# Performance work log

Hardware: AMD Instinct MI355X
Metric: run time of the kernel (lower is better)

Reference implementation:

```python
import jax, jax.numpy as jnp
import numpy as np

D_MODEL = 1024
B, T_Q, T_KV = 4, 2048, 2048


def _linear_params(key, d_in, d_out):
    kw, kb = jax.random.split(key)
    W = jax.random.normal(kw, (d_out, d_in), dtype=jnp.float32) * 0.02
    b = jax.random.normal(kb, (d_out,), dtype=jnp.float32) * 0.02
    return W, b


def setup_inputs() -> dict:
    key = jax.random.key(0)
    ks = jax.random.split(key, 7)
    latent_space = jax.random.normal(ks[0], (B, T_Q, D_MODEL), dtype=jnp.float32)
    input_space = jax.random.normal(ks[1], (B, T_KV, D_MODEL), dtype=jnp.float32)
    Wl, bl = _linear_params(ks[2], D_MODEL, D_MODEL)
    Wu, bu = _linear_params(ks[3], D_MODEL, D_MODEL)
    WA, bA = _linear_params(ks[4], D_MODEL, D_MODEL)  # A_proj: d -> J (J = d)
    WV, bV = _linear_params(ks[5], D_MODEL, D_MODEL)  # V_proj: J -> d
    Wo, bo = _linear_params(ks[6], D_MODEL, D_MODEL)
    return {
        "latent_space": latent_space, "input_space": input_space,
        "Wl": Wl, "bl": bl, "Wu": Wu, "bu": bu,
        "WA": WA, "bA": bA, "WV": WV, "bV": bV,
        "Wo": Wo, "bo": bo,
    }


def reference(latent_space, input_space, Wl, bl, Wu, bu, WA, bA, WV, bV, Wo, bo):
    # emb_0 = l_proj(latent)            [B, T_q, d]
    emb0 = jnp.einsum('bqd,ed->bqe', latent_space, Wl) + bl
    # l = softmax(u_proj(emb_0), -1)^T  [B, d, T_q]
    l = jax.nn.softmax(jnp.einsum('bqd,ed->bqe', emb0, Wu) + bu, axis=-1)
    l = jnp.swapaxes(l, -2, -1)
    # D = A_proj(input)                 [B, T_kv, J]
    Dm = jnp.einsum('bkd,jd->bkj', input_space, WA) + bA
    # A = softmax(V_proj(D), dim=-2)    softmax over T_kv
    A = jax.nn.softmax(jnp.einsum('bkj,dj->bkd', Dm, WV) + bV, axis=-2)
    # w = A @ l                         [B, T_kv, T_q]
    w = jnp.einsum('bkd,bdq->bkq', A, l)
    # o = w @ o_proj(latent)            [B, T_kv, d]
    ov = jnp.einsum('bqd,ed->bqe', latent_space, Wo) + bo
    o = jnp.einsum('bkq,bqd->bkd', w, ov)
    return o
```

## Files before the change

kernel.cpp:

```cpp
#include <hip/hip_runtime.h>
#include <hip/hip_bf16.h>
#include <stdint.h>

typedef __attribute__((ext_vector_type(8))) short bf16x8;
typedef __attribute__((ext_vector_type(4))) float f32x4;
typedef __attribute__((ext_vector_type(4))) unsigned short u16x4;

#define B_  4
#define T_  2048
#define D_  1024
#define BM  128
#define BN  128
#define BK  32

__device__ __forceinline__ float bf2f(ushort u) {
  union { unsigned int i; float f; } v; v.i = ((unsigned int)u) << 16; return v.f;
}
__device__ __forceinline__ ushort f2bf(float f) {
  return (ushort)(__bfloat16_as_ushort(__float2bfloat16(f)));
}
__device__ __forceinline__ void async16(const void* g, void* l) {
  __builtin_amdgcn_global_load_lds(
      (const __attribute__((address_space(1))) void*)g,
      (__attribute__((address_space(3))) void*)l, 16, 0, 0);
}
__device__ __forceinline__ int swz4(int r) { return (r ^ (r >> 2)) & 3; }

__global__ __launch_bounds__(256)
void prep(const float* __restrict__ lat, const float* __restrict__ inp,
          const float* __restrict__ Wl, const float* __restrict__ bl,
          const float* __restrict__ Wu, const float* __restrict__ bu,
          const float* __restrict__ WA, const float* __restrict__ bA,
          const float* __restrict__ WV, const float* __restrict__ bV,
          const float* __restrict__ Wo, const float* __restrict__ bo,
          ushort* __restrict__ xBf, ushort* __restrict__ xBf2,
          ushort* __restrict__ w1, ushort* __restrict__ w2,
          ushort* __restrict__ wCatWo, float* __restrict__ bc, float* __restrict__ bc2)
{
  __shared__ alignas(16) ushort t[64 * 65];
  const long NW = (long)D_ * D_;
  const int bx = blockIdx.x;
  const int tid = threadIdx.x;
  if (bx < 16384) {
    const float* in = bx < 8192 ? lat : inp;
    ushort* out = bx < 8192 ? xBf : xBf2;
    const long i = (long)(bx & 8191) * 256 + tid;
    const float4 v = *(const float4*)(in + i * 4);
    u16x4 o;
    o[0] = f2bf(v.x); o[1] = f2bf(v.y); o[2] = f2bf(v.z); o[3] = f2bf(v.w);
    *(u16x4*)(out + i * 4) = o;
  } else if (bx < 19456) {
    const int seg = (bx - 16384) >> 10;
    const float* in  = seg == 0 ? Wu : (seg == 1 ? WV : Wo);
    ushort* out = seg == 0 ? w1 : (seg == 1 ? w1 + NW : wCatWo);
    const long i = (long)((bx - 16384) & 1023) * 256 + tid;
    const float4 v = *(const float4*)(in + i * 4);
    u16x4 o;
    o[0] = f2bf(v.x); o[1] = f2bf(v.y); o[2] = f2bf(v.z); o[3] = f2bf(v.w);
    *(u16x4*)(out + i * 4) = o;
  } else if (bx < 19968) {
    const int z = (bx - 19456) >> 8;
    const int w = (bx - 19456) & 255;
    const float* in = z ? WA : Wl;
    ushort* out = z ? w2 + NW : w2;
    const int c0 = (w & 15) * 64, r0 = (w >> 4) * 64;
    const int tx = tid & 15, ty = tid >> 4;
#pragma unroll
    for (int i = 0; i < 4; ++i) {
      const int r = ty + i * 16;
      const float4 v = *(const float4*)(in + (long)(r0 + r) * D_ + c0 + tx * 4);
      t[(tx * 4 + 0) * 65 + r] = f2bf(v.x);
      t[(tx * 4 + 1) * 65 + r] = f2bf(v.y);
      t[(tx * 4 + 2) * 65 + r] = f2bf(v.z);
      t[(tx * 4 + 3) * 65 + r] = f2bf(v.w);
    }
    __syncthreads();
#pragma unroll
    for (int i = 0; i < 4; ++i) {
      const int c = ty + i * 16;
      u16x4 v;
#pragma unroll
      for (int j = 0; j < 4; ++j) v[j] = t[c * 65 + tx * 4 + j];
      *(u16x4*)(out + (long)(c0 + c) * D_ + r0 + tx * 4) = v;
    }
  } else {
    const int z = (bx - 19968) >> 8;
    const int w = (bx - 19968) & 255;
    const float* W    = z ? WV : Wu;
    const float* bin  = z ? bA : bl;
    const float* badd = z ? bV : bu;
    float* out        = z ? bc2 : bc;
    const int wv = tid >> 6, lane = tid & 63;
    const int e = w * 4 + wv;
    const float* row = W + (long)e * D_;
    float s = 0.f;
#pragma unroll
    for (int i = 0; i < 16; ++i) s += row[lane + i * 64] * bin[lane + i * 64];
#pragma unroll
    for (int off = 32; off; off >>= 1) s += __shfl_xor(s, off);
    if (lane == 0) out[e] = s + badd[e];
  }
}

template<bool OUT_F32, bool HAS_BIAS, bool EXP_OUT>
__global__ __launch_bounds__(256, 2)
void gemm_nt(const ushort* __restrict__ A, const ushort* __restrict__ B,
             const float* __restrict__ bias, void* __restrict__ C,
             int N, int K, long sA, long sB, long sC)
{
  __shared__ alignas(16) ushort As[BM * BK];
  __shared__ alignas(16) ushort Bs[BN * BK];
  const int tid  = threadIdx.x;
  const int wave = tid >> 6;
  const int lane = tid & 63;
  const int wm   = wave >> 1;
  const int wn   = wave & 1;
  const int bz   = blockIdx.z;
  const int tileN = blockIdx.x * BN;
  const int tileM = blockIdx.y * BM;
  A += (long)bz * sA;
  B += (long)bz * sB;

  const int lrow   = lane >> 2;
  const int lchunk = (lane & 3) ^ swz4(lrow);

  f32x4 acc[4][4];
#pragma unroll
  for (int i = 0; i < 4; ++i)
#pragma unroll
    for (int j = 0; j < 4; ++j) acc[i][j] = (f32x4){0.f, 0.f, 0.f, 0.f};

  const int frow = lane & 15;
  const int kg   = lane >> 4;
  const int coff = ((kg ^ swz4(frow)) << 3);

  for (int kt = 0; kt < K; kt += BK) {
    __syncthreads();
#pragma unroll
    for (int i = 0; i < 2; ++i) {
      const int rg  = wave * 2 + i;
      const int row = rg * 16 + lrow;
      async16(A + (long)(tileM + row) * K + kt + lchunk * 8, (void*)(As + rg * 16 * BK));
      async16(B + (long)(tileN + row) * K + kt + lchunk * 8, (void*)(Bs + rg * 16 * BK));
    }
    __syncthreads();
    bf16x8 af[4], bfr[4];
#pragma unroll
    for (int mi = 0; mi < 4; ++mi)
      af[mi] = *(const bf16x8*)(As + (wm * 64 + mi * 16 + frow) * BK + coff);
#pragma unroll
    for (int ni = 0; ni < 4; ++ni)
      bfr[ni] = *(const bf16x8*)(Bs + (wn * 64 + ni * 16 + frow) * BK + coff);
#pragma unroll
    for (int mi = 0; mi < 4; ++mi)
#pragma unroll
      for (int ni = 0; ni < 4; ++ni)
        acc[mi][ni] = __builtin_amdgcn_mfma_f32_16x16x32_bf16(af[mi], bfr[ni], acc[mi][ni], 0, 0, 0);
  }

  const int rowbase = tileM + wm * 64 + ((lane >> 4) << 2);
  const int colbase = tileN + wn * 64 + (lane & 15);
#pragma unroll
  for (int ni = 0; ni < 4; ++ni) {
    const int col = colbase + ni * 16;
    float bv = 0.f;
    if constexpr (HAS_BIAS) bv = bias[col];
#pragma unroll
    for (int mi = 0; mi < 4; ++mi) {
#pragma unroll
      for (int r = 0; r < 4; ++r) {
        const int row = rowbase + mi * 16 + r;
        float v = acc[mi][ni][r] + bv;
        if constexpr (EXP_OUT) v = __expf(v);
        const long idx = (long)bz * sC + (long)row * N + col;
        if constexpr (OUT_F32) ((float*)C)[idx] = v;
        else ((ushort*)C)[idx] = f2bf(v);
      }
    }
  }
}

__global__ __launch_bounds__(512, 2)
void gemm256(const ushort* __restrict__ A, const ushort* __restrict__ Bm,
             const float* __restrict__ bias1, const float* __restrict__ bias2,
             ushort* __restrict__ C1, ushort* __restrict__ C2,
             int ldA, int ldB)
{
  __shared__ alignas(16) ushort AbS[2 * 16384];
  __shared__ alignas(16) ushort BbS[2 * 16384];

  const int gx = gridDim.x, gy = gridDim.y;
  const int nwg = gx * gy;
  int fid = blockIdx.y * gx + blockIdx.x;
  fid = (fid & 7) * (nwg >> 3) + (fid >> 3);
  const int bx = fid % gx;
  const int by = fid / gx;
  const int tileM = by * 256, tileN = bx * 256;

  const int tid  = threadIdx.x;
  const int wid  = tid >> 6;
  const int lane = tid & 63;
  const int wm   = wid >> 2;
  const int wn   = wid & 3;

  const int srow = tid >> 2;
  const int sc   = (((tid & 3) ^ ((tid >> 3) & 3)) << 3);
  const ushort* gA[2] = { A  + (long)(tileM + srow) * ldA + sc,
                          A  + (long)(tileM + 128 + srow) * ldA + sc };
  const ushort* gB[2] = { Bm + (long)(tileN + srow) * ldB + sc,
                          Bm + (long)(tileN + 128 + srow) * ldB + sc };
  const int dofs = tid << 3;

  const int frow = lane & 15;
  const int cofs = (((lane >> 4) ^ ((lane >> 1) & 3)) << 3);
  int aoff[8], boff[4];
#pragma unroll
  for (int f = 0; f < 8; ++f) {
    const int r = wm * 64 + (f & 3) * 16 + frow;
    aoff[f] = ((f >> 2) << 13) + (r << 5) + cofs;
  }
#pragma unroll
  for (int n = 0; n < 4; ++n) {
    const int row = wn * 64 + n * 16 + frow;
    boff[n] = ((row >> 7) << 13) + ((row & 127) << 5) + cofs;
  }

#define STA256(b, h, kh, kt) async16(gA[h] + (long)(kt) * 64 + (kh) * 32, \
    AbS + (b) * 16384 + (h) * 8192 + (kh) * 4096 + dofs)
#define STB256(b, h, kh, kt) async16(gB[h] + (long)(kt) * 64 + (kh) * 32, \
    BbS + (b) * 16384 + (h) * 8192 + (kh) * 4096 + dofs)

  f32x4 acc[8][4];
#pragma unroll
  for (int i = 0; i < 8; ++i)
#pragma unroll
    for (int j = 0; j < 4; ++j) acc[i][j] = (f32x4){0.f, 0.f, 0.f, 0.f};

#pragma unroll
  for (int p = 0; p < 2; ++p) {
    STA256(p, 0, 0, p); STA256(p, 0, 1, p); STA256(p, 1, 0, p); STA256(p, 1, 1, p);
    STB256(p, 0, 0, p); STB256(p, 0, 1, p); STB256(p, 1, 0, p); STB256(p, 1, 1, p);
  }
  asm volatile("s_waitcnt vmcnt(0)" ::: "memory");
  __builtin_amdgcn_s_barrier();

#pragma unroll 1
  for (int t = 0; t < 16; ++t) {
    const int buf = t & 1;
    const ushort* Ac = AbS + buf * 16384;
    const ushort* Bc = BbS + buf * 16384;
    bf16x8 fa[4], fb[4];

#pragma unroll
    for (int n = 0; n < 4; ++n) fb[n] = *(const bf16x8*)(Bc + boff[n]);
#pragma unroll
    for (int f = 0; f < 4; ++f) fa[f] = *(const bf16x8*)(Ac + aoff[f]);
    if (t == 15) asm volatile("s_waitcnt vmcnt(0)" ::: "memory");
    else         asm volatile("s_waitcnt vmcnt(6)" ::: "memory");
    __builtin_amdgcn_s_barrier();
    __builtin_amdgcn_sched_barrier(0);
    if (t >= 1 && t <= 14) { STA256(buf ^ 1, 1, 0, t + 1); STA256(buf ^ 1, 1, 1, t + 1); }
    __builtin_amdgcn_s_setprio(1);
#pragma unroll
    for (int f = 0; f < 4; ++f)
#pragma unroll
      for (int n = 0; n < 4; ++n)
        acc[f][n] = __builtin_amdgcn_mfma_f32_16x16x32_bf16(fa[f], fb[n], acc[f][n], 0, 0, 0);
    __builtin_amdgcn_s_setprio(0);

    bf16x8 ga[4];
#pragma unroll
    for (int f = 0; f < 4; ++f) ga[f] = *(const bf16x8*)(Ac + aoff[4 + f]);
    __builtin_amdgcn_s_setprio(1);
#pragma unroll
    for (int f = 0; f < 4; ++f)
#pragma unroll
      for (int n = 0; n < 4; ++n)
        acc[4 + f][n] = __builtin_amdgcn_mfma_f32_16x16x32_bf16(ga[f], fb[n], acc[4 + f][n], 0, 0, 0);
    __builtin_amdgcn_s_setprio(0);

#pragma unroll
    for (int n = 0; n < 4; ++n) fb[n] = *(const bf16x8*)(Bc + boff[n] + 4096);
#pragma unroll
    for (int f = 0; f < 4; ++f) fa[f] = *(const bf16x8*)(Ac + aoff[f] + 4096);
    __builtin_amdgcn_s_setprio(1);
#pragma unroll
    for (int f = 0; f < 4; ++f)
#pragma unroll
      for (int n = 0; n < 4; ++n)
        acc[f][n] = __builtin_amdgcn_mfma_f32_16x16x32_bf16(fa[f], fb[n], acc[f][n], 0, 0, 0);
    __builtin_amdgcn_s_setprio(0);

#pragma unroll
    for (int f = 0; f < 4; ++f) ga[f] = *(const bf16x8*)(Ac + aoff[4 + f] + 4096);
    if (t >= 1 && t <= 14) asm volatile("s_waitcnt vmcnt(2)" ::: "memory");
    __builtin_amdgcn_s_barrier();
    __builtin_amdgcn_sched_barrier(0);
    if (t <= 13) {
      STA256(buf, 0, 0, t + 2); STA256(buf, 0, 1, t + 2);
      STB256(buf, 0, 0, t + 2); STB256(buf, 0, 1, t + 2);
      STB256(buf, 1, 0, t + 2); STB256(buf, 1, 1, t + 2);
    }
    __builtin_amdgcn_s_setprio(1);
#pragma unroll
    for (int f = 0; f < 4; ++f)
#pragma unroll
      for (int n = 0; n < 4; ++n)
        acc[4 + f][n] = __builtin_amdgcn_mfma_f32_16x16x32_bf16(ga[f], fb[n], acc[4 + f][n], 0, 0, 0);
    __builtin_amdgcn_s_setprio(0);
  }
#undef STA256
#undef STB256

  const bool second = tileN >= 1024;
  ushort* Cp = second ? C2 : C1;
  const float* bb = second ? bias2 : bias1;
  const int cb = tileN - (second ? 1024 : 0) + wn * 64 + (lane & 15);
#pragma unroll
  for (int mi = 0; mi < 8; ++mi) {
    const int mrow = tileM + wm * 64 + ((mi & 3) << 4) + ((mi >> 2) << 7) + ((lane >> 4) << 2);
#pragma unroll
    for (int ni = 0; ni < 4; ++ni) {
      const int col = cb + ni * 16;
      const float bv = bb[col];
#pragma unroll
      for (int r = 0; r < 4; ++r)
        Cp[(long)(mrow + r) * 1024 + col] = f2bf(acc[mi][ni][r] + bv);
    }
  }
}

template<int MODE>
__global__ __launch_bounds__(512, 2)
void gemm128(const ushort* __restrict__ A, const ushort* __restrict__ Bm,
             const float* __restrict__ bias1, void* __restrict__ C1,
             int ldA, int ldB, long sAz, long sBz, long sCz)
{
  __shared__ alignas(16) ushort AbS[3 * 16384];
  __shared__ alignas(16) ushort BbS[3 * 8192];

  const int gx = gridDim.x, gy = gridDim.y;
  const int nwg = gx * gy * gridDim.z;
  int fid = (blockIdx.z * gy + blockIdx.y) * gx + blockIdx.x;
  fid = (fid & 7) * (nwg >> 3) + (fid >> 3);
  const int bx = fid % gx;
  const int by = (fid / gx) % gy;
  const int bz = fid / (gx * gy);
  const int tileM = by * 256, tileN = bx * 128;

  const ushort* Ap = A;
  const ushort* Bp = Bm;
  if constexpr (MODE == 2) {
    Ap += (long)(bz >> 1) * sAz + (long)(bz & 1) * 1024;
    Bp += (long)(bz >> 1) * sBz + (long)(bz & 1) * 1024;
  } else {
    Ap += (long)bz * sAz;
    Bp += (long)bz * sBz;
  }

  const int tid  = threadIdx.x;
  const int wid  = tid >> 6;
  const int lane = tid & 63;
  const int wm   = wid >> 1;
  const int wn   = wid & 1;

  const int srow = tid >> 2;
  const int sc   = (((tid & 3) ^ ((tid >> 3) & 3)) << 3);
  const ushort* gA[2] = { Ap + (long)(tileM + srow) * ldA + sc,
                          Ap + (long)(tileM + 128 + srow) * ldA + sc };
  const ushort* gB    =   Bp + (long)(tileN + srow) * ldB + sc;
  const int dofs = tid << 3;

  const int frow = lane & 15;
  const int cofs = (((lane >> 4) ^ ((lane >> 1) & 3)) << 3);
  int aoff[4], boff[4];
#pragma unroll
  for (int f = 0; f < 4; ++f) {
    const int row = wm * 64 + f * 16 + frow;
    aoff[f] = ((row >> 7) << 13) + ((row & 127) << 5) + cofs;
  }
#pragma unroll
  for (int n = 0; n < 4; ++n) {
    const int row = wn * 64 + n * 16 + frow;
    boff[n] = (row << 5) + cofs;
  }

#define STA128(b, h, kh, kt) async16(gA[h] + (long)(kt) * 64 + (kh) * 32, \
    AbS + (b) * 16384 + (h) * 8192 + (kh) * 4096 + dofs)
#define STB128(b, kh, kt) async16(gB + (long)(kt) * 64 + (kh) * 32, \
    BbS + (b) * 8192 + (kh) * 4096 + dofs)
#define STAGE_TILE(b, kt) { STA128(b, 0, 0, kt); STA128(b, 0, 1, kt); \
    STA128(b, 1, 0, kt); STA128(b, 1, 1, kt); STB128(b, 0, kt); STB128(b, 1, kt); }

  f32x4 acc[4][4];
#pragma unroll
  for (int i = 0; i < 4; ++i)
#pragma unroll
    for (int j = 0; j < 4; ++j) acc[i][j] = (f32x4){0.f, 0.f, 0.f, 0.f};

  STAGE_TILE(0, 0);
  STAGE_TILE(1, 1);
  asm volatile("s_waitcnt vmcnt(0)" ::: "memory");
  __builtin_amdgcn_s_barrier();

#pragma unroll 1
  for (int t = 0; t < 16; ++t) {
    const int buf = t - (t / 3) * 3;
    const int nb  = (t + 2) - ((t + 2) / 3) * 3;
    const ushort* Ac = AbS + buf * 16384;
    const ushort* Bc = BbS + buf * 8192;
    bf16x8 fa[4], fb[4];

#pragma unroll
    for (int n = 0; n < 4; ++n) fb[n] = *(const bf16x8*)(Bc + boff[n]);
#pragma unroll
    for (int f = 0; f < 4; ++f) fa[f] = *(const bf16x8*)(Ac + aoff[f]);
    __builtin_amdgcn_s_barrier();
    __builtin_amdgcn_sched_barrier(0);
    if (t <= 13) STAGE_TILE(nb, t + 2);
    __builtin_amdgcn_s_setprio(1);
#pragma unroll
    for (int f = 0; f < 4; ++f)
#pragma unroll
      for (int n = 0; n < 4; ++n)
        acc[f][n] = __builtin_amdgcn_mfma_f32_16x16x32_bf16(fa[f], fb[n], acc[f][n], 0, 0, 0);
    __builtin_amdgcn_s_setprio(0);

#pragma unroll
    for (int n = 0; n < 4; ++n) fb[n] = *(const bf16x8*)(Bc + boff[n] + 4096);
#pragma unroll
    for (int f = 0; f < 4; ++f) fa[f] = *(const bf16x8*)(Ac + aoff[f] + 4096);
    if (t <= 13)      asm volatile("s_waitcnt vmcnt(6)" ::: "memory");
    else if (t == 14) asm volatile("s_waitcnt vmcnt(0)" ::: "memory");
    __builtin_amdgcn_s_barrier();
    __builtin_amdgcn_sched_barrier(0);
    __builtin_amdgcn_s_setprio(1);
#pragma unroll
    for (int f = 0; f < 4; ++f)
#pragma unroll
      for (int n = 0; n < 4; ++n)
        acc[f][n] = __builtin_amdgcn_mfma_f32_16x16x32_bf16(fa[f], fb[n], acc[f][n], 0, 0, 0);
    __builtin_amdgcn_s_setprio(0);
  }
#undef STA128
#undef STB128
#undef STAGE_TILE

  const int cb = tileN + wn * 64 + (lane & 15);
  const int rb = tileM + wm * 64 + ((lane >> 4) << 2);

  if constexpr (MODE == 1) {
    ushort* Cp = (ushort*)C1;
#pragma unroll
    for (int ni = 0; ni < 4; ++ni) {
      const int col = cb + ni * 16;
      const float bv = bias1[col];
#pragma unroll
      for (int mi = 0; mi < 4; ++mi)
#pragma unroll
        for (int r = 0; r < 4; ++r)
          Cp[(long)(rb + mi * 16 + r) * 1024 + col] = f2bf(__expf(acc[mi][ni][r] + bv));
    }
  } else if constexpr (MODE == 2) {
    ushort* Cp = (ushort*)C1 + ((long)(bz & 1) * B_ + (bz >> 1)) * ((long)D_ * D_);
#pragma unroll
    for (int ni = 0; ni < 4; ++ni) {
      const int col = cb + ni * 16;
#pragma unroll
      for (int mi = 0; mi < 4; ++mi)
#pragma unroll
        for (int r = 0; r < 4; ++r)
          Cp[(long)(rb + mi * 16 + r) * 1024 + col] = f2bf(acc[mi][ni][r]);
    }
  } else {
    float* Cp = (float*)C1 + (long)bz * sCz;
#pragma unroll
    for (int ni = 0; ni < 4; ++ni) {
      const int col = cb + ni * 16;
#pragma unroll
      for (int mi = 0; mi < 4; ++mi)
#pragma unroll
        for (int r = 0; r < 4; ++r)
          Cp[(long)(rb + mi * 16 + r) * 1024 + col] = acc[mi][ni][r];
    }
  }
}

__global__ __launch_bounds__(256)
void reduce2_scale(const ushort* __restrict__ P, const float* __restrict__ cinv,
                   ushort* __restrict__ MT)
{
  const long stride = (long)B_ * D_ * D_;
  const long base = ((long)blockIdx.x * 256 + threadIdx.x) * 8;
  const int b = (int)(base >> 20);
  const int e0 = (int)(base & (D_ - 1));
  bf16x8 p0 = *(const bf16x8*)(P + base);
  bf16x8 p1 = *(const bf16x8*)(P + stride + base);
  const float4 c0 = *(const float4*)(cinv + (long)b * D_ + e0);
  const float4 c1 = *(const float4*)(cinv + (long)b * D_ + e0 + 4);
  const float cc[8] = {c0.x, c0.y, c0.z, c0.w, c1.x, c1.y, c1.z, c1.w};
  bf16x8 o;
#pragma unroll
  for (int j = 0; j < 8; ++j)
    o[j] = (short)f2bf((bf2f((ushort)p0[j]) + bf2f((ushort)p1[j])) * cc[j]);
  *(bf16x8*)(MT + base) = o;
}

__global__ __launch_bounds__(256)
void softmax_row(ushort* __restrict__ S)
{
  const long base = (long)blockIdx.x * D_;
  const int tid = threadIdx.x;
  float e[4], s = 0.f;
#pragma unroll
  for (int i = 0; i < 4; ++i) { e[i] = __expf(bf2f(S[base + i * 256 + tid])); s += e[i]; }
#pragma unroll
  for (int off = 32; off; off >>= 1) s += __shfl_xor(s, off);
  __shared__ float reds[4];
  if ((tid & 63) == 0) reds[tid >> 6] = s;
  __syncthreads();
  s = reds[0] + reds[1] + reds[2] + reds[3];
  const float inv = 1.f / s;
#pragma unroll
  for (int i = 0; i < 4; ++i)
    S[base + i * 256 + tid] = f2bf(e[i] * inv);
}

__global__ __launch_bounds__(256)
void transpose2(const ushort* __restrict__ l, ushort* __restrict__ lT,
                const ushort* __restrict__ ov, ushort* __restrict__ ovT)
{
  __shared__ alignas(16) ushort t[64 * 65];
  const int z = blockIdx.z;
  const int b = z & (B_ - 1);
  const ushort* in = (z < B_ ? l : ov) + (long)b * T_ * D_;
  ushort* out      = (z < B_ ? lT : ovT) + (long)b * (long)D_ * T_;
  const int c0 = blockIdx.x * 64, r0 = blockIdx.y * 64;
  const int tx = threadIdx.x & 15, ty = threadIdx.x >> 4;
#pragma unroll
  for (int i = 0; i < 4; ++i) {
    const int r = ty + i * 16;
    u16x4 v = *(const u16x4*)(in + (long)(r0 + r) * D_ + c0 + tx * 4);
#pragma unroll
    for (int c = 0; c < 4; ++c) t[(tx * 4 + c) * 65 + r] = v[c];
  }
  __syncthreads();
#pragma unroll
  for (int i = 0; i < 4; ++i) {
    const int c = ty + i * 16;
    u16x4 v;
#pragma unroll
    for (int j = 0; j < 4; ++j) v[j] = t[c * 65 + tx * 4 + j];
    *(u16x4*)(out + (long)(c0 + c) * T_ + r0 + tx * 4) = v;
  }
}

__global__ __launch_bounds__(256)
void colsum_part(const ushort* __restrict__ E, float* __restrict__ psum)
{
  const int d = blockIdx.x * 256 + threadIdx.x;
  const int c = blockIdx.y;
  const int b = blockIdx.z;
  const ushort* p = E + ((long)b * T_ + (long)c * 128) * D_ + d;
  float s = 0.f;
#pragma unroll 4
  for (int r = 0; r < 128; ++r) s += bf2f(p[(long)r * D_]);
  psum[((long)b * 16 + c) * D_ + d] = s;
}

__global__ __launch_bounds__(256)
void colsum_comb(const float* __restrict__ psum, float* __restrict__ cinv)
{
  const int d = blockIdx.x * 256 + threadIdx.x;
  const int b = blockIdx.y;
  float s = 0.f;
#pragma unroll
  for (int c = 0; c < 16; ++c) s += psum[((long)b * 16 + c) * D_ + d];
  cinv[(long)b * D_ + d] = 1.f / s;
}

extern "C" void kernel_launch(void* const* d_in, const int* in_sizes, int n_in,
                              void* d_out, int out_size, void* d_ws, size_t ws_size,
                              hipStream_t stream)
{
  (void)in_sizes; (void)n_in; (void)out_size; (void)ws_size;
  const float* lat = (const float*)d_in[0];
  const float* inp = (const float*)d_in[1];
  const float* Wl  = (const float*)d_in[2];
  const float* bl  = (const float*)d_in[3];
  const float* Wu  = (const float*)d_in[4];
  const float* bu  = (const float*)d_in[5];
  const float* WA  = (const float*)d_in[6];
  const float* bA  = (const float*)d_in[7];
  const float* WV  = (const float*)d_in[8];
  const float* bV  = (const float*)d_in[9];
  const float* Wo  = (const float*)d_in[10];
  const float* bo  = (const float*)d_in[11];

  char* w = (char*)d_ws;
  auto carve = [&](size_t bytes) { char* p = w; w += (bytes + 255) & ~(size_t)255; return p; };
  const long NT = (long)B_ * T_ * D_;
  const long NW = (long)D_ * D_;
  ushort* xBf   = (ushort*)carve(NT * 2);
  ushort* xBf2  = (ushort*)carve(NT * 2);
  ushort* bufA  = (ushort*)carve(NT * 2);
  ushort* bufB  = (ushort*)carve(NT * 2);
  ushort* scr   = (ushort*)carve(NT * 2);
  ushort* MT    = (ushort*)carve((long)B_ * NW * 2);
  ushort* wCat  = (ushort*)carve(3 * NW * 2);
  float*  bc    = (float*)carve(D_ * 4);
  float*  bc2   = (float*)carve(D_ * 4);
  float*  psum  = (float*)carve(64 * 1024 * 4);
  float*  cinv  = (float*)carve(8 * 1024 * 4);
  ushort* w1 = scr;
  ushort* w2 = scr + 2 * NW;
  ushort* ovT = scr;
  ushort* part = bufB;

  const dim3 blk(256, 1, 1);
  const dim3 blk5(512, 1, 1);

  prep<<<dim3(20480), blk, 0, stream>>>(lat, inp, Wl, bl, Wu, bu, WA, bA, WV, bV, Wo, bo,
                                        xBf, xBf2, w1, w2, wCat + NW, bc, bc2);
  gemm_nt<false, false, false><<<dim3(8, 8, 2), blk, 0, stream>>>(
      w1, w2, nullptr, wCat, D_, D_, NW, NW, 2 * NW);
  gemm256<<<dim3(8, 32, 1), blk5, 0, stream>>>(
      xBf, wCat, bc, bo, bufB, bufA, D_, D_);
  softmax_row<<<dim3(B_ * T_), blk, 0, stream>>>(bufB);
  transpose2<<<dim3(16, 32, 2 * B_), blk, 0, stream>>>(bufB, xBf, bufA, ovT);
  gemm128<2><<<dim3(8, 4, 8), blk5, 0, stream>>>(
      ovT, xBf, nullptr, part, T_, T_, (long)D_ * T_, (long)D_ * T_, 0);
  gemm128<1><<<dim3(8, 32, 1), blk5, 0, stream>>>(
      xBf2, wCat + 2 * NW, bc2, bufA, D_, D_, 0, 0, 0);
  colsum_part<<<dim3(4, 16, B_), blk, 0, stream>>>(bufA, psum);
  colsum_comb<<<dim3(4, B_, 1), blk, 0, stream>>>(psum, cinv);
  reduce2_scale<<<dim3(2048), blk, 0, stream>>>(part, cinv, MT);
  gemm128<3><<<dim3(8, 8, 4), blk5, 0, stream>>>(
      bufA, MT, nullptr, d_out, D_, D_,
      (long)T_ * D_, NW, (long)T_ * D_);
}
```

Measured before the change: 323.3 us.

## Restructure GEMM pipelines into half-tile staged loads with phase barriers

Both GEMM kernels now load each K tile as two halves (kh), issuing the next half-tile's async global-to-LDS copies inside the compute phases instead of as whole tiles. Every MFMA phase is bracketed by barrier/lgkmcnt/setprio sync macros. The gemm128 kernel drops from triple to double buffering, which frees LDS, and the gemm256 LDS layout and warp row mapping change so each warp covers 128 contiguous rows. The aim is finer-grained overlap of memory and MFMA work and, for gemm128, possibly higher occupancy. The cost is more barriers per iteration and tighter vmcnt bookkeeping that could stall or race.

After: 321.2 us. Within noise of the previous version (-0.7%).

```diff
diff --git a/kernel.cpp b/kernel.cpp
--- a/kernel.cpp
+++ b/kernel.cpp
@@ -180,6 +180,15 @@
   }
 }
 
+#define PH_SYNC_IN()                                               \
+  __builtin_amdgcn_s_barrier();                                    \
+  asm volatile("s_waitcnt lgkmcnt(0)" ::: "memory");               \
+  __builtin_amdgcn_sched_barrier(0);                               \
+  __builtin_amdgcn_s_setprio(1)
+#define PH_SYNC_OUT()                                              \
+  __builtin_amdgcn_s_setprio(0);                                   \
+  __builtin_amdgcn_s_barrier()
+
 __global__ __launch_bounds__(512, 2)
 void gemm256(const ushort* __restrict__ A, const ushort* __restrict__ Bm,
              const float* __restrict__ bias1, const float* __restrict__ bias2,
@@ -189,8 +198,8 @@
   __shared__ alignas(16) ushort AbS[2 * 16384];
   __shared__ alignas(16) ushort BbS[2 * 16384];
 
-  const int gx = gridDim.x, gy = gridDim.y;
-  const int nwg = gx * gy;
+  const int gx = gridDim.x;
+  const int nwg = gx * gridDim.y;
   int fid = blockIdx.y * gx + blockIdx.x;
   fid = (fid & 7) * (nwg >> 3) + (fid >> 3);
   const int bx = fid % gx;
@@ -205,30 +214,30 @@
 
   const int srow = tid >> 2;
   const int sc   = (((tid & 3) ^ ((tid >> 3) & 3)) << 3);
-  const ushort* gA[2] = { A  + (long)(tileM + srow) * ldA + sc,
-                          A  + (long)(tileM + 128 + srow) * ldA + sc };
-  const ushort* gB[2] = { Bm + (long)(tileN + srow) * ldB + sc,
-                          Bm + (long)(tileN + 128 + srow) * ldB + sc };
+  const ushort* gA0 = A  + (long)(tileM + srow) * ldA + sc;
+  const ushort* gA1 = A  + (long)(tileM + 128 + srow) * ldA + sc;
+  const ushort* gB0 = Bm + (long)(tileN + srow) * ldB + sc;
+  const ushort* gB1 = Bm + (long)(tileN + 128 + srow) * ldB + sc;
   const int dofs = tid << 3;
 
+#define STA(b, kh, t) { \
+    async16(gA0 + (long)(t) * 64 + (kh) * 32, AbS + (b) * 16384 + (kh) * 8192 + dofs); \
+    async16(gA1 + (long)(t) * 64 + (kh) * 32, AbS + (b) * 16384 + (kh) * 8192 + 4096 + dofs); }
+#define STB(b, kh, t) { \
+    async16(gB0 + (long)(t) * 64 + (kh) * 32, BbS + (b) * 16384 + (kh) * 8192 + dofs); \
+    async16(gB1 + (long)(t) * 64 + (kh) * 32, BbS + (b) * 16384 + (kh) * 8192 + 4096 + dofs); }
+
   const int frow = lane & 15;
-  const int cofs = (((lane >> 4) ^ ((lane >> 1) & 3)) << 3);
+  const int cofs = (((lane >> 4) ^ ((frow >> 1) & 3)) << 3);
   int aoff[8], boff[4];
 #pragma unroll
-  for (int f = 0; f < 8; ++f) {
-    const int r = wm * 64 + (f & 3) * 16 + frow;
-    aoff[f] = ((f >> 2) << 13) + (r << 5) + cofs;
-  }
+  for (int mi = 0; mi < 8; ++mi)
+    aoff[mi] = wm * 4096 + (mi * 16 + frow) * 32 + cofs;
 #pragma unroll
   for (int n = 0; n < 4; ++n) {
-    const int row = wn * 64 + n * 16 + frow;
-    boff[n] = ((row >> 7) << 13) + ((row & 127) << 5) + cofs;
-  }
-
-#define STA256(b, h, kh, kt) async16(gA[h] + (long)(kt) * 64 + (kh) * 32, \
-    AbS + (b) * 16384 + (h) * 8192 + (kh) * 4096 + dofs)
-#define STB256(b, h, kh, kt) async16(gB[h] + (long)(kt) * 64 + (kh) * 32, \
-    BbS + (b) * 16384 + (h) * 8192 + (kh) * 4096 + dofs)
+    const int Brow = wn * 64 + n * 16 + frow;
+    boff[n] = (Brow >> 7) * 4096 + (Brow & 127) * 32 + cofs;
+  }
 
   f32x4 acc[8][4];
 #pragma unroll
@@ -236,12 +245,10 @@
 #pragma unroll
     for (int j = 0; j < 4; ++j) acc[i][j] = (f32x4){0.f, 0.f, 0.f, 0.f};
 
-#pragma unroll
-  for (int p = 0; p < 2; ++p) {
-    STA256(p, 0, 0, p); STA256(p, 0, 1, p); STA256(p, 1, 0, p); STA256(p, 1, 1, p);
-    STB256(p, 0, 0, p); STB256(p, 0, 1, p); STB256(p, 1, 0, p); STB256(p, 1, 1, p);
-  }
-  asm volatile("s_waitcnt vmcnt(0)" ::: "memory");
+  STA(0, 0, 0); STB(0, 0, 0);
+  STA(0, 1, 0); STB(0, 1, 0);
+  STA(1, 0, 1); STB(1, 0, 1);
+  asm volatile("s_waitcnt vmcnt(8)" ::: "memory");
   __builtin_amdgcn_s_barrier();
 
 #pragma unroll 1
@@ -249,76 +256,69 @@
     const int buf = t & 1;
     const ushort* Ac = AbS + buf * 16384;
     const ushort* Bc = BbS + buf * 16384;
-    bf16x8 fa[4], fb[4];
+    bf16x8 fa[4], fb[4], ga[4];
 
 #pragma unroll
     for (int n = 0; n < 4; ++n) fb[n] = *(const bf16x8*)(Bc + boff[n]);
 #pragma unroll
-    for (int f = 0; f < 4; ++f) fa[f] = *(const bf16x8*)(Ac + aoff[f]);
-    if (t == 15) asm volatile("s_waitcnt vmcnt(0)" ::: "memory");
-    else         asm volatile("s_waitcnt vmcnt(6)" ::: "memory");
-    __builtin_amdgcn_s_barrier();
-    __builtin_amdgcn_sched_barrier(0);
-    if (t >= 1 && t <= 14) { STA256(buf ^ 1, 1, 0, t + 1); STA256(buf ^ 1, 1, 1, t + 1); }
-    __builtin_amdgcn_s_setprio(1);
-#pragma unroll
-    for (int f = 0; f < 4; ++f)
+    for (int m = 0; m < 4; ++m) fa[m] = *(const bf16x8*)(Ac + aoff[m]);
+    if (t <= 14) { STA(buf ^ 1, 1, t + 1); STB(buf ^ 1, 1, t + 1); }
+    PH_SYNC_IN();
+#pragma unroll
+    for (int m = 0; m < 4; ++m)
 #pragma unroll
       for (int n = 0; n < 4; ++n)
-        acc[f][n] = __builtin_amdgcn_mfma_f32_16x16x32_bf16(fa[f], fb[n], acc[f][n], 0, 0, 0);
-    __builtin_amdgcn_s_setprio(0);
-
-    bf16x8 ga[4];
-#pragma unroll
-    for (int f = 0; f < 4; ++f) ga[f] = *(const bf16x8*)(Ac + aoff[4 + f]);
-    __builtin_amdgcn_s_setprio(1);
-#pragma unroll
-    for (int f = 0; f < 4; ++f)
+        acc[m][n] = __builtin_amdgcn_mfma_f32_16x16x32_bf16(fa[m], fb[n], acc[m][n], 0, 0, 0);
+    PH_SYNC_OUT();
+
+#pragma unroll
+    for (int m = 0; m < 4; ++m) ga[m] = *(const bf16x8*)(Ac + aoff[4 + m]);
+    if (t <= 14) asm volatile("s_waitcnt vmcnt(8)" ::: "memory");
+    else         asm volatile("s_waitcnt vmcnt(0)" ::: "memory");
+    PH_SYNC_IN();
+#pragma unroll
+    for (int m = 0; m < 4; ++m)
 #pragma unroll
       for (int n = 0; n < 4; ++n)
-        acc[4 + f][n] = __builtin_amdgcn_mfma_f32_16x16x32_bf16(ga[f], fb[n], acc[4 + f][n], 0, 0, 0);
-    __builtin_amdgcn_s_setprio(0);
-
-#pragma unroll
-    for (int n = 0; n < 4; ++n) fb[n] = *(const bf16x8*)(Bc + boff[n] + 4096);
-#pragma unroll
-    for (int f = 0; f < 4; ++f) fa[f] = *(const bf16x8*)(Ac + aoff[f] + 4096);
-    __builtin_amdgcn_s_setprio(1);
-#pragma unroll
-    for (int f = 0; f < 4; ++f)
+        acc[4 + m][n] = __builtin_amdgcn_mfma_f32_16x16x32_bf16(ga[m], fb[n], acc[4 + m][n], 0, 0, 0);
+    PH_SYNC_OUT();
+
+#pragma unroll
+    for (int n = 0; n < 4; ++n) fb[n] = *(const bf16x8*)(Bc + boff[n] + 8192);
+#pragma unroll
+    for (int m = 0; m < 4; ++m) fa[m] = *(const bf16x8*)(Ac + aoff[m] + 8192);
+    if (t <= 13) { STA(buf, 0, t + 2); STB(buf, 0, t + 2); }
+    PH_SYNC_IN();
+#pragma unroll
+    for (int m = 0; m < 4; ++m)
 #pragma unroll
       for (int n = 0; n < 4; ++n)
-        acc[f][n] = __builtin_amdgcn_mfma_f32_16x16x32_bf16(fa[f], fb[n], acc[f][n], 0, 0, 0);
-    __builtin_amdgcn_s_setprio(0);
-
-#pragma unroll
-    for (int f = 0; f < 4; ++f) ga[f] = *(const bf16x8*)(Ac + aoff[4 + f] + 4096);
-    if (t >= 1 && t <= 14) asm volatile("s_waitcnt vmcnt(2)" ::: "memory");
-    __builtin_amdgcn_s_barrier();
-    __builtin_amdgcn_sched_barrier(0);
-    if (t <= 13) {
-      STA256(buf, 0, 0, t + 2); STA256(buf, 0, 1, t + 2);
-      STB256(buf, 0, 0, t + 2); STB256(buf, 0, 1, t + 2);
-      STB256(buf, 1, 0, t + 2); STB256(buf, 1, 1, t + 2);
-    }
-    __builtin_amdgcn_s_setprio(1);
-#pragma unroll
-    for (int f = 0; f < 4; ++f)
+        acc[m][n] = __builtin_amdgcn_mfma_f32_16x16x32_bf16(fa[m], fb[n], acc[m][n], 0, 0, 0);
+    PH_SYNC_OUT();
+
+#pragma unroll
+    for (int m = 0; m < 4; ++m) ga[m] = *(const bf16x8*)(Ac + aoff[4 + m] + 8192);
+    if (t <= 13)      asm volatile("s_waitcnt vmcnt(8)" ::: "memory");
+    else if (t == 14) asm volatile("s_waitcnt vmcnt(4)" ::: "memory");
+    PH_SYNC_IN();
+#pragma unroll
+    for (int m = 0; m < 4; ++m)
 #pragma unroll
       for (int n = 0; n < 4; ++n)
-        acc[4 + f][n] = __builtin_amdgcn_mfma_f32_16x16x32_bf16(ga[f], fb[n], acc[4 + f][n], 0, 0, 0);
-    __builtin_amdgcn_s_setprio(0);
-  }
-#undef STA256
-#undef STB256
+        acc[4 + m][n] = __builtin_amdgcn_mfma_f32_16x16x32_bf16(ga[m], fb[n], acc[4 + m][n], 0, 0, 0);
+    PH_SYNC_OUT();
+  }
+#undef STA
+#undef STB
 
   const bool second = tileN >= 1024;
   ushort* Cp = second ? C2 : C1;
   const float* bb = second ? bias2 : bias1;
   const int cb = tileN - (second ? 1024 : 0) + wn * 64 + (lane & 15);
+  const int rb = tileM + wm * 128 + ((lane >> 4) << 2);
 #pragma unroll
   for (int mi = 0; mi < 8; ++mi) {
-    const int mrow = tileM + wm * 64 + ((mi & 3) << 4) + ((mi >> 2) << 7) + ((lane >> 4) << 2);
+    const int mrow = rb + mi * 16;
 #pragma unroll
     for (int ni = 0; ni < 4; ++ni) {
       const int col = cb + ni * 16;
@@ -336,8 +336,8 @@
              const float* __restrict__ bias1, void* __restrict__ C1,
              int ldA, int ldB, long sAz, long sBz, long sCz)
 {
-  __shared__ alignas(16) ushort AbS[3 * 16384];
-  __shared__ alignas(16) ushort BbS[3 * 8192];
+  __shared__ alignas(16) ushort AbS[2 * 16384];
+  __shared__ alignas(16) ushort BbS[2 * 8192];
 
   const int gx = gridDim.x, gy = gridDim.y;
   const int nwg = gx * gy * gridDim.z;
@@ -366,31 +366,28 @@
 
   const int srow = tid >> 2;
   const int sc   = (((tid & 3) ^ ((tid >> 3) & 3)) << 3);
-  const ushort* gA[2] = { Ap + (long)(tileM + srow) * ldA + sc,
-                          Ap + (long)(tileM + 128 + srow) * ldA + sc };
-  const ushort* gB    =   Bp + (long)(tileN + srow) * ldB + sc;
+  const ushort* gA0 = Ap + (long)(tileM + srow) * ldA + sc;
+  const ushort* gA1 = Ap + (long)(tileM + 128 + srow) * ldA + sc;
+  const ushort* gB0 = Bp + (long)(tileN + srow) * ldB + sc;
   const int dofs = tid << 3;
 
+#define STA(b, kh, t) { \
+    async16(gA0 + (long)(t) * 64 + (kh) * 32, AbS + (b) * 16384 + (kh) * 8192 + dofs); \
+    async16(gA1 + (long)(t) * 64 + (kh) * 32, AbS + (b) * 16384 + (kh) * 8192 + 4096 + dofs); }
+#define STB(b, kh, t) \
+    async16(gB0 + (long)(t) * 64 + (kh) * 32, BbS + (b) * 8192 + (kh) * 4096 + dofs);
+
   const int frow = lane & 15;
-  const int cofs = (((lane >> 4) ^ ((lane >> 1) & 3)) << 3);
+  const int cofs = (((lane >> 4) ^ ((frow >> 1) & 3)) << 3);
   int aoff[4], boff[4];
 #pragma unroll
-  for (int f = 0; f < 4; ++f) {
-    const int row = wm * 64 + f * 16 + frow;
-    aoff[f] = ((row >> 7) << 13) + ((row & 127) << 5) + cofs;
-  }
-#pragma unroll
-  for (int n = 0; n < 4; ++n) {
-    const int row = wn * 64 + n * 16 + frow;
-    boff[n] = (row << 5) + cofs;
-  }
-
-#define STA128(b, h, kh, kt) async16(gA[h] + (long)(kt) * 64 + (kh) * 32, \
-    AbS + (b) * 16384 + (h) * 8192 + (kh) * 4096 + dofs)
-#define STB128(b, kh, kt) async16(gB + (long)(kt) * 64 + (kh) * 32, \
-    BbS + (b) * 8192 + (kh) * 4096 + dofs)
-#define STAGE_TILE(b, kt) { STA128(b, 0, 0, kt); STA128(b, 0, 1, kt); \
-    STA128(b, 1, 0, kt); STA128(b, 1, 1, kt); STB128(b, 0, kt); STB128(b, 1, kt); }
+  for (int mi = 0; mi < 4; ++mi) {
+    const int R = wm * 64 + mi * 16 + frow;
+    aoff[mi] = (R >> 7) * 4096 + (R & 127) * 32 + cofs;
+  }
+#pragma unroll
+  for (int n = 0; n < 4; ++n)
+    boff[n] = (wn * 64 + n * 16 + frow) * 32 + cofs;
 
   f32x4 acc[4][4];
 #pragma unroll
@@ -398,15 +395,15 @@
 #pragma unroll
     for (int j = 0; j < 4; ++j) acc[i][j] = (f32x4){0.f, 0.f, 0.f, 0.f};
 
-  STAGE_TILE(0, 0);
-  STAGE_TILE(1, 1);
-  asm volatile("s_waitcnt vmcnt(0)" ::: "memory");
+  STA(0, 0, 0); STB(0, 0, 0);
+  STA(0, 1, 0); STB(0, 1, 0);
+  STA(1, 0, 1); STB(1, 0, 1);
+  asm volatile("s_waitcnt vmcnt(6)" ::: "memory");
   __builtin_amdgcn_s_barrier();
 
 #pragma unroll 1
   for (int t = 0; t < 16; ++t) {
-    const int buf = t - (t / 3) * 3;
-    const int nb  = (t + 2) - ((t + 2) / 3) * 3;
+    const int buf = t & 1;
     const ushort* Ac = AbS + buf * 16384;
     const ushort* Bc = BbS + buf * 8192;
     bf16x8 fa[4], fb[4];
@@ -414,37 +411,35 @@
 #pragma unroll
     for (int n = 0; n < 4; ++n) fb[n] = *(const bf16x8*)(Bc + boff[n]);
 #pragma unroll
-    for (int f = 0; f < 4; ++f) fa[f] = *(const bf16x8*)(Ac + aoff[f]);
-    __builtin_amdgcn_s_barrier();
-    __builtin_amdgcn_sched_barrier(0);
-    if (t <= 13) STAGE_TILE(nb, t + 2);
-    __builtin_amdgcn_s_setprio(1);
-#pragma unroll
-    for (int f = 0; f < 4; ++f)
+    for (int m = 0; m < 4; ++m) fa[m] = *(const bf16x8*)(Ac + aoff[m]);
+    if (t <= 14) { STA(buf ^ 1, 1, t + 1); STB(buf ^ 1, 1, t + 1); }
+    if (t <= 14) asm volatile("s_waitcnt vmcnt(6)" ::: "memory");
+    else         asm volatile("s_waitcnt vmcnt(0)" ::: "memory");
+    PH_SYNC_IN();
+#pragma unroll
+    for (int m = 0; m < 4; ++m)
 #pragma unroll
       for (int n = 0; n < 4; ++n)
-        acc[f][n] = __builtin_amdgcn_mfma_f32_16x16x32_bf16(fa[f], fb[n], acc[f][n], 0, 0, 0);
-    __builtin_amdgcn_s_setprio(0);
+        acc[m][n] = __builtin_amdgcn_mfma_f32_16x16x32_bf16(fa[m], fb[n], acc[m][n], 0, 0, 0);
+    PH_SYNC_OUT();
 
 #pragma unroll
     for (int n = 0; n < 4; ++n) fb[n] = *(const bf16x8*)(Bc + boff[n] + 4096);
 #pragma unroll
-    for (int f = 0; f < 4; ++f) fa[f] = *(const bf16x8*)(Ac + aoff[f] + 4096);
+    for (int m = 0; m < 4; ++m) fa[m] = *(const bf16x8*)(Ac + aoff[m] + 8192);
+    if (t <= 13) { STA(buf, 0, t + 2); STB(buf, 0, t + 2); }
     if (t <= 13)      asm volatile("s_waitcnt vmcnt(6)" ::: "memory");
-    else if (t == 14) asm volatile("s_waitcnt vmcnt(0)" ::: "memory");
-    __builtin_amdgcn_s_barrier();
-    __builtin_amdgcn_sched_barrier(0);
-    __builtin_amdgcn_s_setprio(1);
-#pragma unroll
-    for (int f = 0; f < 4; ++f)
+    else if (t == 14) asm volatile("s_waitcnt vmcnt(3)" ::: "memory");
+    PH_SYNC_IN();
+#pragma unroll
+    for (int m = 0; m < 4; ++m)
 #pragma unroll
       for (int n = 0; n < 4; ++n)
-        acc[f][n] = __builtin_amdgcn_mfma_f32_16x16x32_bf16(fa[f], fb[n], acc[f][n], 0, 0, 0);
-    __builtin_amdgcn_s_setprio(0);
-  }
-#undef STA128
-#undef STB128
-#undef STAGE_TILE
+        acc[m][n] = __builtin_amdgcn_mfma_f32_16x16x32_bf16(fa[m], fb[n], acc[m][n], 0, 0, 0);
+    PH_SYNC_OUT();
+  }
+#undef STA
+#undef STB
 
   const int cb = tileN + wn * 64 + (lane & 15);
   const int rb = tileM + wm * 64 + ((lane >> 4) << 2);
```
